# Kernel tuning notes

Measured on AMD Instinct MI355X. Metric: run time of the kernel, lower is better.

## Reference

```python
import jax, jax.numpy as jnp
import numpy as np

K, D = 512, 64


def setup_inputs() -> dict:
    key = jax.random.key(0)
    k1, k2 = jax.random.split(key)
    z_e_x = jax.random.normal(k1, (32, 4096, D), dtype=jnp.float32)
    # nn.Embedding weight initialized uniform(-1/K, 1/K)
    codebook = jax.random.uniform(k2, (K, D), dtype=jnp.float32,
                                  minval=-1.0 / K, maxval=1.0 / K)
    return {"z_e_x": z_e_x, "codebook": codebook}


def reference(z_e_x, codebook):
    # vq(): pairwise squared L2 distances to codebook, then argmin.
    d = z_e_x.shape[-1]
    flat = z_e_x.reshape(-1, d)                                   # [N, D]
    # ||z||^2 - 2 z.e + ||e||^2  (addmm form from original vq)
    dists = (jnp.sum(flat * flat, axis=1, keepdims=True)
             - 2.0 * flat @ codebook.T
             + jnp.sum(codebook * codebook, axis=1))              # [N, K]
    indices = jnp.argmin(dists, axis=1)                            # [N]
    # latents: indices reshaped to input shape minus feature dim
    return indices.reshape(z_e_x.shape[:-1])
```

## Files before the change

### kernel.cpp

```cpp
#include <hip/hip_runtime.h>
#include <math.h>

#define K_CODES 512
#define D_DIM   64
#define BM      256
#define THREADS 256
#define LSTR    72
#define EPS_GAP 4e-5f

#define WS_CNT_OFF  2048
#define WS_EH_OFF   4096
#define WS_EL_OFF   77824
#define WS_LIST_OFF 151552

typedef __attribute__((ext_vector_type(8))) short short8v;
typedef __attribute__((ext_vector_type(4))) float f32x4;

__device__ __forceinline__ float np_sumsq64(const float* zarr) {
    float L[16];
#pragma unroll
    for (int j = 0; j < 16; ++j)
        L[j] = __fadd_rn(
            __fadd_rn(__fmul_rn(zarr[j],      zarr[j]),
                      __fmul_rn(zarr[j + 16], zarr[j + 16])),
            __fadd_rn(__fmul_rn(zarr[j + 32], zarr[j + 32]),
                      __fmul_rn(zarr[j + 48], zarr[j + 48])));
    float m[8];
#pragma unroll
    for (int j = 0; j < 8; ++j) m[j] = __fadd_rn(L[j], L[j + 8]);
    float n4[4];
#pragma unroll
    for (int j = 0; j < 4; ++j) n4[j] = __fadd_rn(m[j], m[j + 4]);
    return __fadd_rn(__fadd_rn(n4[0], n4[2]), __fadd_rn(n4[1], n4[3]));
}

__device__ __forceinline__ unsigned short f32_bf16_rne(float x) {
    unsigned int u = __float_as_uint(x);
    unsigned int r = (u + 0x7FFFu + ((u >> 16) & 1u)) >> 16;
    return (unsigned short)r;
}
__device__ __forceinline__ float bf16_f32(unsigned short h) {
    return __uint_as_float(((unsigned int)h) << 16);
}
__device__ __forceinline__ void split2(float x, unsigned short& h, unsigned short& l) {
    h = f32_bf16_rne(x);
    l = f32_bf16_rne(x - bf16_f32(h));
}

__global__ __launch_bounds__(256)
void vq_prep_kernel(const float* __restrict__ cb, float* __restrict__ ws,
                    int do_split) {
    int k = blockIdx.x * blockDim.x + threadIdx.x;
    if (k == 0) *reinterpret_cast<int*>((char*)ws + WS_CNT_OFF) = 0;
    if (k >= K_CODES) return;
    float e[D_DIM];
    const float4* p = reinterpret_cast<const float4*>(cb + (size_t)k * D_DIM);
#pragma unroll
    for (int i = 0; i < 16; ++i) {
        float4 v = p[i];
        e[4*i+0]=v.x; e[4*i+1]=v.y; e[4*i+2]=v.z; e[4*i+3]=v.w;
    }
    ws[k] = np_sumsq64(e);
    if (do_split) {
        unsigned short* eh = reinterpret_cast<unsigned short*>((char*)ws + WS_EH_OFF)
                             + (size_t)k * LSTR;
        unsigned short* el = reinterpret_cast<unsigned short*>((char*)ws + WS_EL_OFF)
                             + (size_t)k * LSTR;
#pragma unroll
        for (int i = 0; i < D_DIM; ++i) {
            unsigned short h, l;
            split2(e[i], h, l);
            eh[i] = h; el[i] = l;
        }
#pragma unroll
        for (int i = D_DIM; i < LSTR; ++i) { eh[i] = 0; el[i] = 0; }
    }
}

__global__ __launch_bounds__(256)
void vq_pass1_stream(const float* __restrict__ z,
                     const unsigned short* __restrict__ eh_g,
                     const unsigned short* __restrict__ el_g,
                     const float* __restrict__ norms, int* __restrict__ out,
                     int* __restrict__ cnt, int* __restrict__ list, int cap, int n) {
    const int tid  = threadIdx.x;
    const int l    = tid & 63;
    const int w    = tid >> 6;
    const int j    = l >> 4;
    const int c16  = l & 15;
    const int base = blockIdx.x * BM;

    short8v bzh[4][2], bzl[4][2];
#pragma unroll
    for (int p = 0; p < 4; ++p) {
        int row = base + (4 * w + p) * 16 + c16;
        if (row >= n) row = n - 1;
        const float* zp = z + (size_t)row * D_DIM + j * 8;
#pragma unroll
        for (int h = 0; h < 2; ++h) {
            float4 v0 = *reinterpret_cast<const float4*>(zp + h * 32);
            float4 v1 = *reinterpret_cast<const float4*>(zp + h * 32 + 4);
            unsigned short hh[8], ll[8];
            split2(v0.x, hh[0], ll[0]); split2(v0.y, hh[1], ll[1]);
            split2(v0.z, hh[2], ll[2]); split2(v0.w, hh[3], ll[3]);
            split2(v1.x, hh[4], ll[4]); split2(v1.y, hh[5], ll[5]);
            split2(v1.z, hh[6], ll[6]); split2(v1.w, hh[7], ll[7]);
            short8v th, tl;
#pragma unroll
            for (int i = 0; i < 8; ++i) { th[i] = (short)hh[i]; tl[i] = (short)ll[i]; }
            bzh[p][h] = th; bzl[p][h] = tl;
        }
    }

    float m1[4] = {INFINITY, INFINITY, INFINITY, INFINITY};
    float m2[4] = {INFINITY, INFINITY, INFINITY, INFINITY};
    int   i1[4] = {0, 0, 0, 0};

#pragma unroll 8
    for (int ct = 0; ct < 32; ++ct) {
        const unsigned short* er = eh_g + (size_t)(ct * 16 + c16) * LSTR + j * 8;
        const unsigned short* lr = el_g + (size_t)(ct * 16 + c16) * LSTR + j * 8;
        short8v aeh0 = *reinterpret_cast<const short8v*>(er);
        short8v aeh1 = *reinterpret_cast<const short8v*>(er + 32);
        short8v ael0 = *reinterpret_cast<const short8v*>(lr);
        short8v ael1 = *reinterpret_cast<const short8v*>(lr + 32);
        float4 nr = *reinterpret_cast<const float4*>(norms + ct * 16 + j * 4);
        float nra[4] = {nr.x, nr.y, nr.z, nr.w};
        int kg0 = ct * 16 + j * 4;
#pragma unroll
        for (int p = 0; p < 4; ++p) {
            f32x4 acc = {0.f, 0.f, 0.f, 0.f};
            acc = __builtin_amdgcn_mfma_f32_16x16x32_bf16(aeh0, bzh[p][0], acc, 0, 0, 0);
            acc = __builtin_amdgcn_mfma_f32_16x16x32_bf16(aeh1, bzh[p][1], acc, 0, 0, 0);
            acc = __builtin_amdgcn_mfma_f32_16x16x32_bf16(aeh0, bzl[p][0], acc, 0, 0, 0);
            acc = __builtin_amdgcn_mfma_f32_16x16x32_bf16(aeh1, bzl[p][1], acc, 0, 0, 0);
            acc = __builtin_amdgcn_mfma_f32_16x16x32_bf16(ael0, bzh[p][0], acc, 0, 0, 0);
            acc = __builtin_amdgcn_mfma_f32_16x16x32_bf16(ael1, bzh[p][1], acc, 0, 0, 0);
#pragma unroll
            for (int r = 0; r < 4; ++r) {
                float s = fmaf(-2.0f, acc[r], nra[r]);
                int kg = kg0 + r;
                bool lt1 = s < m1[p];
                float nm2 = lt1 ? m1[p] : fminf(s, m2[p]);
                i1[p] = lt1 ? kg : i1[p];
                m1[p] = lt1 ? s : m1[p];
                m2[p] = nm2;
            }
        }
    }

#pragma unroll
    for (int p = 0; p < 4; ++p) {
        float a1 = m1[p], a2 = m2[p]; int ai = i1[p];
#pragma unroll
        for (int off = 16; off <= 32; off <<= 1) {
            float o1 = __shfl_xor(a1, off, 64);
            float o2 = __shfl_xor(a2, off, 64);
            int   oi = __shfl_xor(ai, off, 64);
            float hi = fmaxf(a1, o1);
            bool take = o1 < a1;
            ai = take ? oi : ai;
            a1 = take ? o1 : a1;
            a2 = fminf(hi, fminf(a2, o2));
        }
        int  ptg    = base + (4 * w + p) * 16 + c16;
        bool writer = (j == 0) && (ptg < n);
        bool flag   = writer && (a2 - a1 <= EPS_GAP);
        unsigned long long m = __ballot(flag);
        int abase = 0;
        if (m) {
            int leader = __ffsll(m) - 1;
            if (l == leader) abase = atomicAdd(cnt, __popcll(m));
            abase = __shfl(abase, leader, 64);
        }
        if (writer) {
            int val = ai;
            if (flag) {
                int rank = __popcll(m & ((1ull << l) - 1ull));
                int slot = abase + rank;
                if (slot < cap) list[slot] = ptg;
                else            val |= (int)0x80000000;
            }
            out[ptg] = val;
        }
    }
}

__global__ __launch_bounds__(256)
void vq_pass1_legacy(const float* __restrict__ z, const float* __restrict__ cb,
                     const float* __restrict__ norms, int* __restrict__ out,
                     int* __restrict__ cnt, int* __restrict__ list, int cap, int n) {
    __shared__ unsigned short zhS[128 * LSTR];
    __shared__ unsigned short zlS[128 * LSTR];
    __shared__ unsigned short ehS[128 * LSTR];
    __shared__ unsigned short elS[128 * LSTR];
    __shared__ float nrmL[128];

    const int tid  = threadIdx.x;
    const int l    = tid & 63;
    const int w    = tid >> 6;
    const int j    = l >> 4;
    const int c16  = l & 15;
    const int base = blockIdx.x * 128;

    const float4* z4 = reinterpret_cast<const float4*>(z);
#pragma unroll
    for (int rep = 0; rep < 8; ++rep) {
        int flat = rep * THREADS + tid;
        int pt   = flat >> 4;
        int dblk = flat & 15;
        int gp = base + pt; if (gp >= n) gp = n - 1;
        float4 v = z4[(size_t)gp * 16 + dblk];
        ushort4 h, lo;
        split2(v.x, h.x, lo.x); split2(v.y, h.y, lo.y);
        split2(v.z, h.z, lo.z); split2(v.w, h.w, lo.w);
        *reinterpret_cast<ushort4*>(&zhS[pt * LSTR + dblk * 4]) = h;
        *reinterpret_cast<ushort4*>(&zlS[pt * LSTR + dblk * 4]) = lo;
    }
    __syncthreads();

    short8v bzh[2][2], bzl[2][2];
#pragma unroll
    for (int p = 0; p < 2; ++p) {
        int pr = ((2 * w + p) * 16 + c16) * LSTR;
#pragma unroll
        for (int h = 0; h < 2; ++h) {
            int off = pr + h * 32 + j * 8;
            bzh[p][h] = *reinterpret_cast<const short8v*>(&zhS[off]);
            bzl[p][h] = *reinterpret_cast<const short8v*>(&zlS[off]);
        }
    }

    float m1[2] = {INFINITY, INFINITY};
    float m2[2] = {INFINITY, INFINITY};
    int   i1[2] = {0, 0};

    for (int c = 0; c < 4; ++c) {
        __syncthreads();
        const float4* cb4 = reinterpret_cast<const float4*>(cb);
#pragma unroll
        for (int rep = 0; rep < 8; ++rep) {
            int flat = rep * THREADS + tid;
            int code = flat >> 4;
            int dblk = flat & 15;
            float4 v = cb4[(size_t)(c * 128 + code) * 16 + dblk];
            ushort4 h, lo;
            split2(v.x, h.x, lo.x); split2(v.y, h.y, lo.y);
            split2(v.z, h.z, lo.z); split2(v.w, h.w, lo.w);
            *reinterpret_cast<ushort4*>(&ehS[code * LSTR + dblk * 4]) = h;
            *reinterpret_cast<ushort4*>(&elS[code * LSTR + dblk * 4]) = lo;
        }
        if (tid < 32)
            reinterpret_cast<float4*>(nrmL)[tid] =
                reinterpret_cast<const float4*>(norms)[c * 32 + tid];
        __syncthreads();

#pragma unroll
        for (int ct = 0; ct < 8; ++ct) {
            int ar = (ct * 16 + c16) * LSTR + j * 8;
            short8v aeh0 = *reinterpret_cast<const short8v*>(&ehS[ar]);
            short8v aeh1 = *reinterpret_cast<const short8v*>(&ehS[ar + 32]);
            short8v ael0 = *reinterpret_cast<const short8v*>(&elS[ar]);
            short8v ael1 = *reinterpret_cast<const short8v*>(&elS[ar + 32]);
            float4 nr = *reinterpret_cast<const float4*>(&nrmL[ct * 16 + j * 4]);
            float nra[4] = {nr.x, nr.y, nr.z, nr.w};
            int kg0 = c * 128 + ct * 16 + j * 4;
#pragma unroll
            for (int p = 0; p < 2; ++p) {
                f32x4 acc = {0.f, 0.f, 0.f, 0.f};
                acc = __builtin_amdgcn_mfma_f32_16x16x32_bf16(aeh0, bzh[p][0], acc, 0, 0, 0);
                acc = __builtin_amdgcn_mfma_f32_16x16x32_bf16(aeh1, bzh[p][1], acc, 0, 0, 0);
                acc = __builtin_amdgcn_mfma_f32_16x16x32_bf16(aeh0, bzl[p][0], acc, 0, 0, 0);
                acc = __builtin_amdgcn_mfma_f32_16x16x32_bf16(aeh1, bzl[p][1], acc, 0, 0, 0);
                acc = __builtin_amdgcn_mfma_f32_16x16x32_bf16(ael0, bzh[p][0], acc, 0, 0, 0);
                acc = __builtin_amdgcn_mfma_f32_16x16x32_bf16(ael1, bzh[p][1], acc, 0, 0, 0);
#pragma unroll
                for (int r = 0; r < 4; ++r) {
                    float s = fmaf(-2.0f, acc[r], nra[r]);
                    int kg = kg0 + r;
                    bool lt1 = s < m1[p];
                    float nm2 = lt1 ? m1[p] : fminf(s, m2[p]);
                    i1[p] = lt1 ? kg : i1[p];
                    m1[p] = lt1 ? s : m1[p];
                    m2[p] = nm2;
                }
            }
        }
    }

#pragma unroll
    for (int p = 0; p < 2; ++p) {
        float a1 = m1[p], a2 = m2[p]; int ai = i1[p];
#pragma unroll
        for (int off = 16; off <= 32; off <<= 1) {
            float o1 = __shfl_xor(a1, off, 64);
            float o2 = __shfl_xor(a2, off, 64);
            int   oi = __shfl_xor(ai, off, 64);
            float hi = fmaxf(a1, o1);
            bool take = o1 < a1;
            ai = take ? oi : ai;
            a1 = take ? o1 : a1;
            a2 = fminf(hi, fminf(a2, o2));
        }
        int  ptg    = base + (2 * w + p) * 16 + c16;
        bool writer = (j == 0) && (ptg < n);
        bool flag   = writer && (a2 - a1 <= EPS_GAP);
        unsigned long long m = __ballot(flag);
        int abase = 0;
        if (m) {
            int leader = __ffsll(m) - 1;
            if (l == leader) abase = atomicAdd(cnt, __popcll(m));
            abase = __shfl(abase, leader, 64);
        }
        if (writer) {
            int val = ai;
            if (flag) {
                int rank = __popcll(m & ((1ull << l) - 1ull));
                int slot = abase + rank;
                if (slot < cap) list[slot] = ptg;
                else            val |= (int)0x80000000;
            }
            out[ptg] = val;
        }
    }
}

__device__ __forceinline__ void vq_rescan_point(
        const float* __restrict__ z, const float* __restrict__ cb,
        const float* __restrict__ norms, int* __restrict__ out,
        int pt, int lane) {
    float zr[D_DIM];
    const float4* zp = reinterpret_cast<const float4*>(z + (size_t)pt * D_DIM);
#pragma unroll
    for (int i = 0; i < 16; ++i) {
        float4 q = zp[i];
        zr[4*i+0]=q.x; zr[4*i+1]=q.y; zr[4*i+2]=q.z; zr[4*i+3]=q.w;
    }
    const float sz = np_sumsq64(zr);
    float best = INFINITY; int bi = 0x7FFFFFFF;
#pragma unroll 1
    for (int r = 0; r < 8; ++r) {
        const float4* e4 = reinterpret_cast<const float4*>(cb) +
                           ((size_t)(lane * 8 + r) << 4);
        float a = 0.f;
#pragma unroll
        for (int g = 0; g < 16; ++g) {
            float4 q = e4[g];
            a = fmaf(zr[4*g+0], q.x, a);
            a = fmaf(zr[4*g+1], q.y, a);
            a = fmaf(zr[4*g+2], q.z, a);
            a = fmaf(zr[4*g+3], q.w, a);
        }
        float s = __fadd_rn(__fsub_rn(sz, __fmul_rn(2.0f, a)),
                            norms[lane * 8 + r]);
        if (s < best) { best = s; bi = lane * 8 + r; }
    }
#pragma unroll
    for (int off = 1; off < 64; off <<= 1) {
        float os = __shfl_xor(best, off, 64);
        int   ok = __shfl_xor(bi, off, 64);
        if (os < best || (os == best && ok < bi)) { best = os; bi = ok; }
    }
    if (lane == 0) out[pt] = bi;
}

__global__ __launch_bounds__(256)
void vq_cleanup_kernel(const float* __restrict__ z, const float* __restrict__ cb,
                       const float* __restrict__ norms,
                       const int* __restrict__ cnt, const int* __restrict__ list,
                       int cap, int* __restrict__ out, int n) {
    const int lane   = threadIdx.x & 63;
    const int wid    = (blockIdx.x * blockDim.x + threadIdx.x) >> 6;
    const int nwaves = (gridDim.x * blockDim.x) >> 6;

    int total = *cnt;
    int lim   = total < cap ? total : cap;
    for (int i = wid; i < lim; i += nwaves)
        vq_rescan_point(z, cb, norms, out, list[i], lane);

    if (total > cap) {
        for (int b = wid * 64; b < n; b += nwaves * 64) {
            int t = b + lane;
            int v = (t < n) ? out[t] : 0;
            unsigned long long m = __ballot(v < 0);
            while (m) {
                int bb = __ffsll(m) - 1;
                m &= m - 1ull;
                vq_rescan_point(z, cb, norms, out, b + bb, lane);
            }
        }
    }
}

extern "C" void kernel_launch(void* const* d_in, const int* in_sizes, int n_in,
                              void* d_out, int out_size, void* d_ws, size_t ws_size,
                              hipStream_t stream) {
    const float* z  = (const float*)d_in[0];
    const float* cb = (const float*)d_in[1];
    int n = in_sizes[0] / D_DIM;
    float* norms = (float*)d_ws;
    int*   cnt   = (int*)((char*)d_ws + WS_CNT_OFF);
    int* out = (int*)d_out;

    bool fast = ws_size >= (size_t)WS_LIST_OFF + 4096;
    vq_prep_kernel<<<(K_CODES + 255) / 256, 256, 0, stream>>>(cb, norms, fast ? 1 : 0);

    if (fast) {
        const unsigned short* eh = (const unsigned short*)((char*)d_ws + WS_EH_OFF);
        const unsigned short* el = (const unsigned short*)((char*)d_ws + WS_EL_OFF);
        int* list = (int*)((char*)d_ws + WS_LIST_OFF);
        int  cap  = (int)((ws_size - WS_LIST_OFF) / 4);
        vq_pass1_stream<<<(n + BM - 1) / BM, THREADS, 0, stream>>>(
            z, eh, el, norms, out, cnt, list, cap, n);
        vq_cleanup_kernel<<<512, 256, 0, stream>>>(z, cb, norms, cnt, list, cap, out, n);
    } else {
        int* list = (int*)d_ws + 513;
        int  cap  = (int)(ws_size / 4) - 513; if (cap < 0) cap = 0;
        vq_pass1_legacy<<<(n + 127) / 128, THREADS, 0, stream>>>(
            z, cb, norms, out, cnt, list, cap, n);
        vq_cleanup_kernel<<<512, 256, 0, stream>>>(z, cb, norms, cnt, list, cap, out, n);
    }
}
```

Measured before the change: 75.49 us.

## Stage split codebook in LDS via async loads, widen blocks, parallelize prep and cleanup

```diff
diff --git a/kernel.cpp b/kernel.cpp
--- a/kernel.cpp
+++ b/kernel.cpp
@@ -3,8 +3,8 @@
 
 #define K_CODES 512
 #define D_DIM   64
-#define BM      256
-#define THREADS 256
+#define BM      512
+#define THREADS 512
 #define LSTR    72
 #define EPS_GAP 4e-5f
 
@@ -50,45 +50,72 @@
 __global__ __launch_bounds__(256)
 void vq_prep_kernel(const float* __restrict__ cb, float* __restrict__ ws,
                     int do_split) {
-    int k = blockIdx.x * blockDim.x + threadIdx.x;
-    if (k == 0) *reinterpret_cast<int*>((char*)ws + WS_CNT_OFF) = 0;
+    int g = blockIdx.x * blockDim.x + threadIdx.x;
+    if (g == 0) *reinterpret_cast<int*>((char*)ws + WS_CNT_OFF) = 0;
+    int k = g >> 2, q = g & 3;
     if (k >= K_CODES) return;
-    float e[D_DIM];
-    const float4* p = reinterpret_cast<const float4*>(cb + (size_t)k * D_DIM);
-#pragma unroll
-    for (int i = 0; i < 16; ++i) {
-        float4 v = p[i];
-        e[4*i+0]=v.x; e[4*i+1]=v.y; e[4*i+2]=v.z; e[4*i+3]=v.w;
-    }
-    ws[k] = np_sumsq64(e);
+    const float* row = cb + (size_t)k * D_DIM;
+    if (q == 0) {
+        float e[D_DIM];
+        const float4* p = reinterpret_cast<const float4*>(row);
+#pragma unroll
+        for (int i = 0; i < 16; ++i) {
+            float4 v = p[i];
+            e[4*i+0]=v.x; e[4*i+1]=v.y; e[4*i+2]=v.z; e[4*i+3]=v.w;
+        }
+        ws[k] = np_sumsq64(e);
+    }
     if (do_split) {
         unsigned short* eh = reinterpret_cast<unsigned short*>((char*)ws + WS_EH_OFF)
                              + (size_t)k * LSTR;
         unsigned short* el = reinterpret_cast<unsigned short*>((char*)ws + WS_EL_OFF)
                              + (size_t)k * LSTR;
 #pragma unroll
-        for (int i = 0; i < D_DIM; ++i) {
+        for (int i = 16 * q; i < 16 * q + 16; ++i) {
             unsigned short h, l;
-            split2(e[i], h, l);
+            split2(row[i], h, l);
             eh[i] = h; el[i] = l;
         }
-#pragma unroll
-        for (int i = D_DIM; i < LSTR; ++i) { eh[i] = 0; el[i] = 0; }
-    }
-}
-
-__global__ __launch_bounds__(256)
-void vq_pass1_stream(const float* __restrict__ z,
-                     const unsigned short* __restrict__ eh_g,
-                     const unsigned short* __restrict__ el_g,
-                     const float* __restrict__ norms, int* __restrict__ out,
-                     int* __restrict__ cnt, int* __restrict__ list, int cap, int n) {
+        if (q == 3)
+#pragma unroll
+            for (int i = D_DIM; i < LSTR; ++i) { eh[i] = 0; el[i] = 0; }
+    }
+}
+
+__global__ __launch_bounds__(512)
+void vq_pass1_mono(const float* __restrict__ z,
+                   const unsigned short* __restrict__ eh_g,
+                   const unsigned short* __restrict__ el_g,
+                   const float* __restrict__ norms, int* __restrict__ out,
+                   int* __restrict__ cnt, int* __restrict__ list, int cap, int n) {
+    __shared__ __align__(16) unsigned short ehS[K_CODES * LSTR];
+    __shared__ __align__(16) unsigned short elS[K_CODES * LSTR];
+    __shared__ __align__(16) float nrmS[K_CODES];
+
     const int tid  = threadIdx.x;
     const int l    = tid & 63;
     const int w    = tid >> 6;
     const int j    = l >> 4;
     const int c16  = l & 15;
     const int base = blockIdx.x * BM;
+
+    {
+        const char* esrc = (const char*)eh_g;
+        const char* lsrc = (const char*)el_g;
+#pragma unroll
+        for (int r = 0; r < 9; ++r) {
+            size_t off = ((size_t)tid + (size_t)r * THREADS) * 16;
+            __builtin_amdgcn_global_load_lds(
+                (const __attribute__((address_space(1))) void*)(esrc + off),
+                (__attribute__((address_space(3))) void*)((char*)ehS + off), 16, 0, 0);
+            __builtin_amdgcn_global_load_lds(
+                (const __attribute__((address_space(1))) void*)(lsrc + off),
+                (__attribute__((address_space(3))) void*)((char*)elS + off), 16, 0, 0);
+        }
+        if (tid < K_CODES / 4)
+            reinterpret_cast<float4*>(nrmS)[tid] =
+                reinterpret_cast<const float4*>(norms)[tid];
+    }
 
     short8v bzh[4][2], bzl[4][2];
 #pragma unroll
@@ -112,19 +139,20 @@
         }
     }
 
+    __syncthreads();
+
     float m1[4] = {INFINITY, INFINITY, INFINITY, INFINITY};
     float m2[4] = {INFINITY, INFINITY, INFINITY, INFINITY};
     int   i1[4] = {0, 0, 0, 0};
 
-#pragma unroll 8
+#pragma unroll 4
     for (int ct = 0; ct < 32; ++ct) {
-        const unsigned short* er = eh_g + (size_t)(ct * 16 + c16) * LSTR + j * 8;
-        const unsigned short* lr = el_g + (size_t)(ct * 16 + c16) * LSTR + j * 8;
-        short8v aeh0 = *reinterpret_cast<const short8v*>(er);
-        short8v aeh1 = *reinterpret_cast<const short8v*>(er + 32);
-        short8v ael0 = *reinterpret_cast<const short8v*>(lr);
-        short8v ael1 = *reinterpret_cast<const short8v*>(lr + 32);
-        float4 nr = *reinterpret_cast<const float4*>(norms + ct * 16 + j * 4);
+        int ar = (ct * 16 + c16) * LSTR + j * 8;
+        short8v aeh0 = *reinterpret_cast<const short8v*>(&ehS[ar]);
+        short8v aeh1 = *reinterpret_cast<const short8v*>(&ehS[ar + 32]);
+        short8v ael0 = *reinterpret_cast<const short8v*>(&elS[ar]);
+        short8v ael1 = *reinterpret_cast<const short8v*>(&elS[ar + 32]);
+        float4 nr = *reinterpret_cast<const float4*>(&nrmS[ct * 16 + j * 4]);
         float nra[4] = {nr.x, nr.y, nr.z, nr.w};
         int kg0 = ct * 16 + j * 4;
 #pragma unroll
@@ -206,7 +234,7 @@
     const float4* z4 = reinterpret_cast<const float4*>(z);
 #pragma unroll
     for (int rep = 0; rep < 8; ++rep) {
-        int flat = rep * THREADS + tid;
+        int flat = rep * 256 + tid;
         int pt   = flat >> 4;
         int dblk = flat & 15;
         int gp = base + pt; if (gp >= n) gp = n - 1;
@@ -240,7 +268,7 @@
         const float4* cb4 = reinterpret_cast<const float4*>(cb);
 #pragma unroll
         for (int rep = 0; rep < 8; ++rep) {
-            int flat = rep * THREADS + tid;
+            int flat = rep * 256 + tid;
             int code = flat >> 4;
             int dblk = flat & 15;
             float4 v = cb4[(size_t)(c * 128 + code) * 16 + dblk];
@@ -325,60 +353,70 @@
     }
 }
 
-__device__ __forceinline__ void vq_rescan_point(
-        const float* __restrict__ z, const float* __restrict__ cb,
-        const float* __restrict__ norms, int* __restrict__ out,
-        int pt, int lane) {
-    float zr[D_DIM];
-    const float4* zp = reinterpret_cast<const float4*>(z + (size_t)pt * D_DIM);
-#pragma unroll
-    for (int i = 0; i < 16; ++i) {
-        float4 q = zp[i];
-        zr[4*i+0]=q.x; zr[4*i+1]=q.y; zr[4*i+2]=q.z; zr[4*i+3]=q.w;
-    }
-    const float sz = np_sumsq64(zr);
-    float best = INFINITY; int bi = 0x7FFFFFFF;
-#pragma unroll 1
-    for (int r = 0; r < 8; ++r) {
-        const float4* e4 = reinterpret_cast<const float4*>(cb) +
-                           ((size_t)(lane * 8 + r) << 4);
-        float a = 0.f;
-#pragma unroll
-        for (int g = 0; g < 16; ++g) {
-            float4 q = e4[g];
-            a = fmaf(zr[4*g+0], q.x, a);
-            a = fmaf(zr[4*g+1], q.y, a);
-            a = fmaf(zr[4*g+2], q.z, a);
-            a = fmaf(zr[4*g+3], q.w, a);
-        }
-        float s = __fadd_rn(__fsub_rn(sz, __fmul_rn(2.0f, a)),
-                            norms[lane * 8 + r]);
-        if (s < best) { best = s; bi = lane * 8 + r; }
-    }
-#pragma unroll
-    for (int off = 1; off < 64; off <<= 1) {
-        float os = __shfl_xor(best, off, 64);
-        int   ok = __shfl_xor(bi, off, 64);
-        if (os < best || (os == best && ok < bi)) { best = os; bi = ok; }
-    }
-    if (lane == 0) out[pt] = bi;
-}
-
 __global__ __launch_bounds__(256)
 void vq_cleanup_kernel(const float* __restrict__ z, const float* __restrict__ cb,
                        const float* __restrict__ norms,
                        const int* __restrict__ cnt, const int* __restrict__ list,
                        int cap, int* __restrict__ out, int n) {
-    const int lane   = threadIdx.x & 63;
-    const int wid    = (blockIdx.x * blockDim.x + threadIdx.x) >> 6;
-    const int nwaves = (gridDim.x * blockDim.x) >> 6;
+    __shared__ float rbv[4];
+    __shared__ int   rbi[4];
+    const int tid  = threadIdx.x;
+    const int lane = tid & 63;
+    const int wv   = tid >> 6;
 
     int total = *cnt;
     int lim   = total < cap ? total : cap;
-    for (int i = wid; i < lim; i += nwaves)
-        vq_rescan_point(z, cb, norms, out, list[i], lane);
+
+    for (int i = blockIdx.x; i < lim; i += gridDim.x) {
+        int pt = list[i];
+        float zr[D_DIM];
+        const float4* zp = reinterpret_cast<const float4*>(z + (size_t)pt * D_DIM);
+#pragma unroll
+        for (int g = 0; g < 16; ++g) {
+            float4 q = zp[g];
+            zr[4*g+0]=q.x; zr[4*g+1]=q.y; zr[4*g+2]=q.z; zr[4*g+3]=q.w;
+        }
+        const float sz = np_sumsq64(zr);
+        float best = INFINITY; int bi = 0x7FFFFFFF;
+#pragma unroll 1
+        for (int r = 0; r < 2; ++r) {
+            int k = tid * 2 + r;
+            const float4* e4 = reinterpret_cast<const float4*>(cb) + ((size_t)k << 4);
+            float a = 0.f;
+#pragma unroll
+            for (int g = 0; g < 16; ++g) {
+                float4 q = e4[g];
+                a = fmaf(zr[4*g+0], q.x, a);
+                a = fmaf(zr[4*g+1], q.y, a);
+                a = fmaf(zr[4*g+2], q.z, a);
+                a = fmaf(zr[4*g+3], q.w, a);
+            }
+            float s = __fadd_rn(__fsub_rn(sz, __fmul_rn(2.0f, a)), norms[k]);
+            if (s < best || (s == best && k < bi)) { best = s; bi = k; }
+        }
+#pragma unroll
+        for (int off = 1; off < 64; off <<= 1) {
+            float os = __shfl_xor(best, off, 64);
+            int   ok = __shfl_xor(bi, off, 64);
+            if (os < best || (os == best && ok < bi)) { best = os; bi = ok; }
+        }
+        if (lane == 0) { rbv[wv] = best; rbi[wv] = bi; }
+        __syncthreads();
+        if (tid == 0) {
+            float b = rbv[0]; int id = rbi[0];
+#pragma unroll
+            for (int q = 1; q < 4; ++q) {
+                float v = rbv[q]; int vi = rbi[q];
+                if (v < b || (v == b && vi < id)) { b = v; id = vi; }
+            }
+            out[pt] = id;
+        }
+        __syncthreads();
+    }
 
     if (total > cap) {
+        const int wid    = (blockIdx.x * blockDim.x + tid) >> 6;
+        const int nwaves = (gridDim.x * blockDim.x) >> 6;
         for (int b = wid * 64; b < n; b += nwaves * 64) {
             int t = b + lane;
             int v = (t < n) ? out[t] : 0;
@@ -386,7 +424,40 @@
             while (m) {
                 int bb = __ffsll(m) - 1;
                 m &= m - 1ull;
-                vq_rescan_point(z, cb, norms, out, b + bb, lane);
+                int pt = b + bb;
+                float zr[D_DIM];
+                const float4* zp = reinterpret_cast<const float4*>(z + (size_t)pt * D_DIM);
+#pragma unroll
+                for (int g = 0; g < 16; ++g) {
+                    float4 q = zp[g];
+                    zr[4*g+0]=q.x; zr[4*g+1]=q.y; zr[4*g+2]=q.z; zr[4*g+3]=q.w;
+                }
+                const float sz = np_sumsq64(zr);
+                float best = INFINITY; int bi = 0x7FFFFFFF;
+#pragma unroll 1
+                for (int r = 0; r < 8; ++r) {
+                    const float4* e4 = reinterpret_cast<const float4*>(cb) +
+                                       ((size_t)(lane * 8 + r) << 4);
+                    float a = 0.f;
+#pragma unroll
+                    for (int g = 0; g < 16; ++g) {
+                        float4 q = e4[g];
+                        a = fmaf(zr[4*g+0], q.x, a);
+                        a = fmaf(zr[4*g+1], q.y, a);
+                        a = fmaf(zr[4*g+2], q.z, a);
+                        a = fmaf(zr[4*g+3], q.w, a);
+                    }
+                    float s = __fadd_rn(__fsub_rn(sz, __fmul_rn(2.0f, a)),
+                                        norms[lane * 8 + r]);
+                    if (s < best) { best = s; bi = lane * 8 + r; }
+                }
+#pragma unroll
+                for (int off = 1; off < 64; off <<= 1) {
+                    float os = __shfl_xor(best, off, 64);
+                    int   ok = __shfl_xor(bi, off, 64);
+                    if (os < best || (os == best && ok < bi)) { best = os; bi = ok; }
+                }
+                if (lane == 0) out[pt] = bi;
             }
         }
     }
@@ -403,21 +474,21 @@
     int* out = (int*)d_out;
 
     bool fast = ws_size >= (size_t)WS_LIST_OFF + 4096;
-    vq_prep_kernel<<<(K_CODES + 255) / 256, 256, 0, stream>>>(cb, norms, fast ? 1 : 0);
+    vq_prep_kernel<<<(4 * K_CODES + 255) / 256, 256, 0, stream>>>(cb, norms, fast ? 1 : 0);
 
     if (fast) {
         const unsigned short* eh = (const unsigned short*)((char*)d_ws + WS_EH_OFF);
         const unsigned short* el = (const unsigned short*)((char*)d_ws + WS_EL_OFF);
         int* list = (int*)((char*)d_ws + WS_LIST_OFF);
         int  cap  = (int)((ws_size - WS_LIST_OFF) / 4);
-        vq_pass1_stream<<<(n + BM - 1) / BM, THREADS, 0, stream>>>(
+        vq_pass1_mono<<<(n + BM - 1) / BM, THREADS, 0, stream>>>(
             z, eh, el, norms, out, cnt, list, cap, n);
-        vq_cleanup_kernel<<<512, 256, 0, stream>>>(z, cb, norms, cnt, list, cap, out, n);
+        vq_cleanup_kernel<<<2048, 256, 0, stream>>>(z, cb, norms, cnt, list, cap, out, n);
     } else {
         int* list = (int*)d_ws + 513;
         int  cap  = (int)(ws_size / 4) - 513; if (cap < 0) cap = 0;
-        vq_pass1_legacy<<<(n + 127) / 128, THREADS, 0, stream>>>(
+        vq_pass1_legacy<<<(n + 127) / 128, 256, 0, stream>>>(
             z, cb, norms, out, cnt, list, cap, n);
-        vq_cleanup_kernel<<<512, 256, 0, stream>>>(z, cb, norms, cnt, list, cap, out, n);
-    }
-}
+        vq_cleanup_kernel<<<2048, 256, 0, stream>>>(z, cb, norms, cnt, list, cap, out, n);
+    }
+}
```

New measurement: 61.00 us. 19.2% less time.
